# Optimization experiments

Hardware: AMD Instinct MI355X
Metric: run time of the kernel (lower is better)

## Reference

```python
import jax, jax.numpy as jnp
import numpy as np
from jax import lax

B, D, K = 65536, 256, 32  # batch, num_latent_dims, flow_depth


def setup_inputs() -> dict:
    key = jax.random.key(0)
    k1, k2, k3, k4, k5 = jax.random.split(key, 5)
    X = jax.random.normal(k1, (B, D), dtype=jnp.float32)
    h = jax.random.normal(k2, (B, D), dtype=jnp.float32)  # passed through, unused by planar math
    u = jax.random.normal(k3, (K, D), dtype=jnp.float32) * 0.1
    w = jax.random.normal(k4, (K, D), dtype=jnp.float32) * 0.1
    b = jax.random.normal(k5, (K,), dtype=jnp.float32) * 0.1
    return {"X": X, "h": h, "u": u, "w": w, "b": b}


def _planar_chain(z0, u, w, b):
    """Sequential planar normalizing flow: z_{k+1} = z_k + u_hat_k * tanh(w_k.z_k + b_k)."""

    def step(z, params):
        u_k, w_k, b_k = params  # (D,), (D,), scalar
        # enforce invertibility: u_hat so that w.u_hat >= -1
        wu = jnp.dot(w_k, u_k)
        u_hat = u_k + (jax.nn.softplus(wu) - 1.0 - wu) * w_k / jnp.dot(w_k, w_k)
        lin = z @ w_k + b_k              # (B,)
        t = jnp.tanh(lin)                # (B,)
        z_new = z + t[:, None] * u_hat[None, :]
        # psi = (1 - t^2) w ; log|det J| = log|1 + psi.u_hat|
        log_det = jnp.log(jnp.abs(1.0 + (1.0 - t * t) * jnp.dot(w_k, u_hat)) + 1e-8)
        return z_new, log_det

    z_final, log_dets = lax.scan(step, z0, (u, w, b))
    return z_final, log_dets  # (B, D), (K, B)


def reference(X, h, u, w, b):
    z = X.reshape(X.shape[0], X.shape[1])  # view(B, D, -1) then view(B, D) -> (B, D)
    z_final, log_det_jacobians = _planar_chain(z, u, w, b)
    return z_final, log_det_jacobians
```

## Files before the change

kernel.cpp:

```cpp
#include <hip/hip_runtime.h>


#define B_ 65536
#define D_ 256
#define ROWS 128
#define GRID (B_ / ROWS)

#define WS_WT 0
#define WS_UH 8192
#define WS_G  16384
#define WS_C  17408

#define P_STR 132
#define T_OFF 4224
#define G_OFF 8448
#define C_OFF 9504
#define BB_OFF 9536
#define LDS_FLOATS 9568

__global__ __launch_bounds__(256) void nf_gen(const float* __restrict__ u_in,
                                              const float* __restrict__ w_in,
                                              float* __restrict__ ws) {
  __shared__ float wTg[8192];
  __shared__ float ug[8192];
  __shared__ float wu_s[32], ww_s[32], coefs_s[32];
  const int t = threadIdx.x;
  {
    const int k = t & 31, d0 = (t >> 5) * 32;
    const float4* wp = (const float4*)(w_in + k * 256 + d0);
#pragma unroll
    for (int q = 0; q < 8; ++q) {
      float4 v = wp[q];
      wTg[(d0 + q * 4 + 0) * 32 + k] = v.x;
      wTg[(d0 + q * 4 + 1) * 32 + k] = v.y;
      wTg[(d0 + q * 4 + 2) * 32 + k] = v.z;
      wTg[(d0 + q * 4 + 3) * 32 + k] = v.w;
    }
#pragma unroll
    for (int q = 0; q < 8; ++q)
      ((float4*)ug)[t + 256 * q] = ((const float4*)u_in)[t + 256 * q];
  }
  __syncthreads();
  const int k = t & 31, jg = t >> 5;
  float m1[4] = {0.f, 0.f, 0.f, 0.f}, m2[4] = {0.f, 0.f, 0.f, 0.f};
#pragma unroll 4
  for (int dc = 0; dc < 64; ++dc) {
    float wk[4];
    float4 wj[4], uj[4];
#pragma unroll
    for (int i = 0; i < 4; ++i) wk[i] = wTg[(dc * 4 + i) * 32 + k];
#pragma unroll
    for (int i = 0; i < 4; ++i) wj[i] = *(const float4*)&wTg[(dc * 4 + i) * 32 + jg * 4];
#pragma unroll
    for (int i = 0; i < 4; ++i) uj[i] = *(const float4*)&ug[(jg * 4 + i) * 256 + dc * 4];
#pragma unroll
    for (int i = 0; i < 4; ++i) {
      m1[i] = fmaf(uj[i].x, wk[0], m1[i]);
      m1[i] = fmaf(uj[i].y, wk[1], m1[i]);
      m1[i] = fmaf(uj[i].z, wk[2], m1[i]);
      m1[i] = fmaf(uj[i].w, wk[3], m1[i]);
    }
    const float* w0 = (const float*)&wj[0];
    const float* w1 = (const float*)&wj[1];
    const float* w2 = (const float*)&wj[2];
    const float* w3 = (const float*)&wj[3];
#pragma unroll
    for (int i = 0; i < 4; ++i) {
      m2[i] = fmaf(w0[i], wk[0], m2[i]);
      m2[i] = fmaf(w1[i], wk[1], m2[i]);
      m2[i] = fmaf(w2[i], wk[2], m2[i]);
      m2[i] = fmaf(w3[i], wk[3], m2[i]);
    }
  }
  if ((k >> 2) == jg) {
    wu_s[k] = m1[k & 3];
    ww_s[k] = m2[k & 3];
  }
  __syncthreads();
  if (t < 32) {
    float wu = wu_s[t], ww = ww_s[t];
    float sp = fmaxf(wu, 0.f) + log1pf(__expf(-fabsf(wu)));
    coefs_s[t] = (sp - 1.f - wu) / ww;
    ws[WS_C + t] = sp - 1.f;
  }
  __syncthreads();
#pragma unroll
  for (int i = 0; i < 4; ++i)
    ws[WS_G + k * 32 + jg * 4 + i] = fmaf(coefs_s[jg * 4 + i], m2[i], m1[i]);
  {
    const int k2 = t >> 3, d0 = (t & 7) * 32;
    const float ck = coefs_s[k2];
    const float4* up = (const float4*)(u_in + k2 * 256 + d0);
    const float4* wp2 = (const float4*)(w_in + k2 * 256 + d0);
    float4* od = (float4*)(ws + WS_UH + k2 * 256 + d0);
#pragma unroll
    for (int q = 0; q < 8; ++q) {
      float4 uv = up[q], wv = wp2[q];
      uv.x = fmaf(ck, wv.x, uv.x);
      uv.y = fmaf(ck, wv.y, uv.y);
      uv.z = fmaf(ck, wv.z, uv.z);
      uv.w = fmaf(ck, wv.w, uv.w);
      od[q] = uv;
    }
  }
#pragma unroll
  for (int q = 0; q < 8; ++q)
    ((float4*)(ws + WS_WT))[t + 256 * q] = ((const float4*)wTg)[t + 256 * q];
}

__global__ __launch_bounds__(256) void nf_fused(const float* __restrict__ X,
                                                const float* __restrict__ b_in,
                                                const float* __restrict__ ws,
                                                float* __restrict__ out) {
  __shared__ float lds[LDS_FLOATS];

  const int t = threadIdx.x;
  const int row0 = blockIdx.x * ROWS;
  const int xoff = (t >> 6) * 32 + ((t >> 3) & 7) * 4;
  const int kq4 = (t & 7) * 4;
  const int cq8 = (t & 7) * 8;

  float p[4][4];
#pragma unroll
  for (int a = 0; a < 4; ++a)
#pragma unroll
    for (int b2 = 0; b2 < 4; ++b2) p[a][b2] = 0.f;
  {
    const float* wbase = ws + WS_WT + kq4;
    const float* xb = X + (size_t)(row0 + xoff) * 256;
#pragma unroll 2
    for (int dq = 0; dq < 64; ++dq) {
      float4 wr[4];
#pragma unroll
      for (int i = 0; i < 4; ++i) wr[i] = *(const float4*)(wbase + (dq * 4 + i) * 32);
      float4 xr[4];
#pragma unroll
      for (int a = 0; a < 4; ++a) xr[a] = *(const float4*)(xb + a * 256 + dq * 4);
#pragma unroll
      for (int a = 0; a < 4; ++a) {
        const float xf[4] = {xr[a].x, xr[a].y, xr[a].z, xr[a].w};
#pragma unroll
        for (int i = 0; i < 4; ++i) {
          p[a][0] = fmaf(xf[i], wr[i].x, p[a][0]);
          p[a][1] = fmaf(xf[i], wr[i].y, p[a][1]);
          p[a][2] = fmaf(xf[i], wr[i].z, p[a][2]);
          p[a][3] = fmaf(xf[i], wr[i].w, p[a][3]);
        }
      }
    }
  }

#pragma unroll
  for (int b2 = 0; b2 < 4; ++b2)
    *(float4*)&lds[(kq4 + b2) * P_STR + xoff] =
        make_float4(p[0][b2], p[1][b2], p[2][b2], p[3][b2]);
#pragma unroll
  for (int i = 0; i < 4; ++i) {
    const int e = t * 4 + i;
    lds[G_OFF + (e >> 5) * 33 + (e & 31)] = ws[WS_G + e];
  }
  if (t < 32) {
    lds[C_OFF + t] = ws[WS_C + t];
    lds[BB_OFF + t] = b_in[t];
  }
  __syncthreads();

  if (t < 128) {
    float pfull[32];
#pragma unroll
    for (int j = 0; j < 32; ++j) pfull[j] = lds[j * P_STR + t] + lds[BB_OFF + j];
    float tvv[32];
#pragma unroll
    for (int kk = 0; kk < 32; ++kk) {
      float la = pfull[kk], lb = 0.f;
      const float* gp = &lds[G_OFF + kk * 33];
#pragma unroll
      for (int j = 0; j + 1 < kk; j += 2) {
        la = fmaf(tvv[j], gp[j], la);
        lb = fmaf(tvv[j + 1], gp[j + 1], lb);
      }
      if (kk & 1) la = fmaf(tvv[kk - 1], gp[kk - 1], la);
      float lin = la + lb;
      float e = __expf(2.f * lin);
      float tk = 1.f - 2.f / (e + 1.f);
      tvv[kk] = tk;
      lds[T_OFF + kk * P_STR + t] = tk;
      float val = fabsf(fmaf(1.f - tk * tk, lds[C_OFF + kk], 1.f)) + 1e-8f;
      out[(size_t)B_ * D_ + (size_t)kk * B_ + row0 + t] = __logf(val);
    }
  }
  __syncthreads();

  for (int cbk = 0; cbk < 4; ++cbk) {
    const int c0 = cbk * 64 + cq8;
    float acc[4][8];
#pragma unroll
    for (int a = 0; a < 4; ++a) {
      const float4 x0 = *(const float4*)(X + (size_t)(row0 + xoff + a) * 256 + c0);
      const float4 x1 = *(const float4*)(X + (size_t)(row0 + xoff + a) * 256 + c0 + 4);
      acc[a][0] = x0.x; acc[a][1] = x0.y; acc[a][2] = x0.z; acc[a][3] = x0.w;
      acc[a][4] = x1.x; acc[a][5] = x1.y; acc[a][6] = x1.z; acc[a][7] = x1.w;
    }
#pragma unroll 4
    for (int kk = 0; kk < 32; ++kk) {
      float4 t4 = *(const float4*)&lds[T_OFF + kk * P_STR + xoff];
      float4 u0 = *(const float4*)(ws + WS_UH + kk * 256 + c0);
      float4 u1 = *(const float4*)(ws + WS_UH + kk * 256 + c0 + 4);
      const float tr[4] = {t4.x, t4.y, t4.z, t4.w};
      const float uk[8] = {u0.x, u0.y, u0.z, u0.w, u1.x, u1.y, u1.z, u1.w};
#pragma unroll
      for (int a = 0; a < 4; ++a)
#pragma unroll
        for (int b2 = 0; b2 < 8; ++b2) acc[a][b2] = fmaf(tr[a], uk[b2], acc[a][b2]);
    }
#pragma unroll
    for (int a = 0; a < 4; ++a) {
      float4* op = (float4*)(out + (size_t)(row0 + xoff + a) * 256 + c0);
      op[0] = make_float4(acc[a][0], acc[a][1], acc[a][2], acc[a][3]);
      op[1] = make_float4(acc[a][4], acc[a][5], acc[a][6], acc[a][7]);
    }
  }
}

extern "C" void kernel_launch(void* const* d_in, const int* in_sizes, int n_in,
                              void* d_out, int out_size, void* d_ws, size_t ws_size,
                              hipStream_t stream) {
  const float* X = (const float*)d_in[0];
  const float* u = (const float*)d_in[2];
  const float* w = (const float*)d_in[3];
  const float* b = (const float*)d_in[4];
  float* out = (float*)d_out;
  float* ws = (float*)d_ws;

  nf_gen<<<1, 256, 0, stream>>>(u, w, ws);
  nf_fused<<<GRID, 256, 0, stream>>>(X, b, ws, out);
}
```

Measured before the change: 223.8 us.

## Restructure fused planar flow kernel to 128 threads with LDS-staged X tiles

The fused kernel now runs with 128 threads per block. Each wave owns 16 flow columns and each lane owns 2 rows. X is staged through LDS in 32-column slabs using a swizzled transposed layout, with register prefetch of the next slab. The weight, G, coefficient and bias values are read directly from global memory as wave-uniform, likely scalar, loads instead of being copied into LDS. The aim is to cut redundant global X loads and LDS traffic, at the cost of fewer threads per block and many more accumulator registers, which may limit occupancy.

```diff
diff --git a/kernel.cpp b/kernel.cpp
--- a/kernel.cpp
+++ b/kernel.cpp
@@ -5,18 +5,16 @@
 #define D_ 256
 #define ROWS 128
 #define GRID (B_ / ROWS)
+#define NTHR 128
 
 #define WS_WT 0
 #define WS_UH 8192
 #define WS_G  16384
 #define WS_C  17408
 
-#define P_STR 132
-#define T_OFF 4224
-#define G_OFF 8448
-#define C_OFF 9504
-#define BB_OFF 9536
-#define LDS_FLOATS 9568
+#define XS 0
+#define TS 0
+#define PS 4096
 
 __global__ __launch_bounds__(256) void nf_gen(const float* __restrict__ u_in,
                                               const float* __restrict__ w_in,
@@ -108,72 +106,85 @@
     ((float4*)(ws + WS_WT))[t + 256 * q] = ((const float4*)wTg)[t + 256 * q];
 }
 
-__global__ __launch_bounds__(256) void nf_fused(const float* __restrict__ X,
-                                                const float* __restrict__ b_in,
-                                                const float* __restrict__ ws,
-                                                float* __restrict__ out) {
-  __shared__ float lds[LDS_FLOATS];
+__global__ __launch_bounds__(NTHR, 2) void nf_fused(const float* __restrict__ X,
+                                                    const float* __restrict__ b_in,
+                                                    const float* __restrict__ ws,
+                                                    float* __restrict__ out) {
+  __shared__ float lds[8192];
 
   const int t = threadIdx.x;
+  const int lane = t & 63;
+  const int wvu = __builtin_amdgcn_readfirstlane(t >> 6);
   const int row0 = blockIdx.x * ROWS;
-  const int xoff = (t >> 6) * 32 + ((t >> 3) & 7) * 4;
-  const int kq4 = (t & 7) * 4;
-  const int cq8 = (t & 7) * 8;
-
-  float p[4][4];
-#pragma unroll
-  for (int a = 0; a < 4; ++a)
-#pragma unroll
-    for (int b2 = 0; b2 < 4; ++b2) p[a][b2] = 0.f;
-  {
-    const float* wbase = ws + WS_WT + kq4;
-    const float* xb = X + (size_t)(row0 + xoff) * 256;
-#pragma unroll 2
-    for (int dq = 0; dq < 64; ++dq) {
-      float4 wr[4];
-#pragma unroll
-      for (int i = 0; i < 4; ++i) wr[i] = *(const float4*)(wbase + (dq * 4 + i) * 32);
-      float4 xr[4];
-#pragma unroll
-      for (int a = 0; a < 4; ++a) xr[a] = *(const float4*)(xb + a * 256 + dq * 4);
-#pragma unroll
-      for (int a = 0; a < 4; ++a) {
-        const float xf[4] = {xr[a].x, xr[a].y, xr[a].z, xr[a].w};
-#pragma unroll
-        for (int i = 0; i < 4; ++i) {
-          p[a][0] = fmaf(xf[i], wr[i].x, p[a][0]);
-          p[a][1] = fmaf(xf[i], wr[i].y, p[a][1]);
-          p[a][2] = fmaf(xf[i], wr[i].z, p[a][2]);
-          p[a][3] = fmaf(xf[i], wr[i].w, p[a][3]);
-        }
-      }
-    }
-  }
-
-#pragma unroll
-  for (int b2 = 0; b2 < 4; ++b2)
-    *(float4*)&lds[(kq4 + b2) * P_STR + xoff] =
-        make_float4(p[0][b2], p[1][b2], p[2][b2], p[3][b2]);
-#pragma unroll
-  for (int i = 0; i < 4; ++i) {
-    const int e = t * 4 + i;
-    lds[G_OFF + (e >> 5) * 33 + (e & 31)] = ws[WS_G + e];
-  }
-  if (t < 32) {
-    lds[C_OFF + t] = ws[WS_C + t];
-    lds[BB_OFF + t] = b_in[t];
-  }
-  __syncthreads();
-
-  if (t < 128) {
+  const int r2 = 2 * lane;
+  const int srow = t >> 2;
+  const int scol = (t & 3) * 8;
+
+  float4 pf[8];
+  auto load_stage = [&](int s) {
+#pragma unroll
+    for (int rp = 0; rp < 4; ++rp) {
+      const float* src = X + (size_t)(row0 + rp * 32 + srow) * 256 + s * 32 + scol;
+      pf[rp * 2 + 0] = ((const float4*)src)[0];
+      pf[rp * 2 + 1] = ((const float4*)src)[1];
+    }
+  };
+  auto store_stage = [&]() {
+#pragma unroll
+    for (int rp = 0; rp < 4; ++rp) {
+      const int row = rp * 32 + srow;
+      const float f[8] = {pf[rp * 2].x,     pf[rp * 2].y,     pf[rp * 2].z,
+                          pf[rp * 2].w,     pf[rp * 2 + 1].x, pf[rp * 2 + 1].y,
+                          pf[rp * 2 + 1].z, pf[rp * 2 + 1].w};
+#pragma unroll
+      for (int i = 0; i < 8; ++i) {
+        const int c = scol + i;
+        lds[XS + c * 128 + ((row + 6 * c) & 127)] = f[i];
+      }
+    }
+  };
+
+  float p0[16], p1[16];
+#pragma unroll
+  for (int i = 0; i < 16; ++i) { p0[i] = 0.f; p1[i] = 0.f; }
+
+  load_stage(0);
+  const float* wtab = ws + WS_WT + wvu * 16;
+  for (int s = 0; s < 8; ++s) {
+    store_stage();
+    __syncthreads();
+    if (s < 7) load_stage(s + 1);
+#pragma unroll 4
+    for (int dl = 0; dl < 32; ++dl) {
+      const int d = s * 32 + dl;
+      float2 xv = *(const float2*)&lds[XS + dl * 128 + ((r2 + 6 * dl) & 127)];
+      const float* wk = wtab + d * 32;
+#pragma unroll
+      for (int i = 0; i < 16; ++i) {
+        p0[i] = fmaf(xv.x, wk[i], p0[i]);
+        p1[i] = fmaf(xv.y, wk[i], p1[i]);
+      }
+    }
+    __syncthreads();
+  }
+
+  {
+    const int kb = wvu * 16;
+#pragma unroll
+    for (int i = 0; i < 16; ++i)
+      *(float2*)&lds[PS + (kb + i) * 128 + r2] = make_float2(p0[i], p1[i]);
+  }
+  __syncthreads();
+
+  {
     float pfull[32];
 #pragma unroll
-    for (int j = 0; j < 32; ++j) pfull[j] = lds[j * P_STR + t] + lds[BB_OFF + j];
+    for (int j = 0; j < 32; ++j) pfull[j] = lds[PS + j * 128 + t] + b_in[j];
     float tvv[32];
 #pragma unroll
     for (int kk = 0; kk < 32; ++kk) {
       float la = pfull[kk], lb = 0.f;
-      const float* gp = &lds[G_OFF + kk * 33];
+      const float* gp = ws + WS_G + kk * 32;
 #pragma unroll
       for (int j = 0; j + 1 < kk; j += 2) {
         la = fmaf(tvv[j], gp[j], la);
@@ -184,40 +195,48 @@
       float e = __expf(2.f * lin);
       float tk = 1.f - 2.f / (e + 1.f);
       tvv[kk] = tk;
-      lds[T_OFF + kk * P_STR + t] = tk;
-      float val = fabsf(fmaf(1.f - tk * tk, lds[C_OFF + kk], 1.f)) + 1e-8f;
+      lds[TS + kk * 128 + t] = tk;
+      float val = fabsf(fmaf(1.f - tk * tk, ws[WS_C + kk], 1.f)) + 1e-8f;
       out[(size_t)B_ * D_ + (size_t)kk * B_ + row0 + t] = __logf(val);
     }
   }
   __syncthreads();
 
-  for (int cbk = 0; cbk < 4; ++cbk) {
-    const int c0 = cbk * 64 + cq8;
-    float acc[4][8];
-#pragma unroll
-    for (int a = 0; a < 4; ++a) {
-      const float4 x0 = *(const float4*)(X + (size_t)(row0 + xoff + a) * 256 + c0);
-      const float4 x1 = *(const float4*)(X + (size_t)(row0 + xoff + a) * 256 + c0 + 4);
-      acc[a][0] = x0.x; acc[a][1] = x0.y; acc[a][2] = x0.z; acc[a][3] = x0.w;
-      acc[a][4] = x1.x; acc[a][5] = x1.y; acc[a][6] = x1.z; acc[a][7] = x1.w;
-    }
-#pragma unroll 4
+  const float* uws = ws + WS_UH;
+  for (int ps = 0; ps < 4; ++ps) {
+    const int c0 = ps * 64 + wvu * 32;
+    float a0[32], a1[32];
+    {
+      const float* x0 = X + (size_t)(row0 + r2) * 256 + c0;
+      const float* x1 = X + (size_t)(row0 + r2 + 1) * 256 + c0;
+#pragma unroll
+      for (int q = 0; q < 8; ++q) {
+        float4 v0 = ((const float4*)x0)[q];
+        float4 v1 = ((const float4*)x1)[q];
+        a0[q * 4 + 0] = v0.x; a0[q * 4 + 1] = v0.y;
+        a0[q * 4 + 2] = v0.z; a0[q * 4 + 3] = v0.w;
+        a1[q * 4 + 0] = v1.x; a1[q * 4 + 1] = v1.y;
+        a1[q * 4 + 2] = v1.z; a1[q * 4 + 3] = v1.w;
+      }
+    }
+#pragma unroll 2
     for (int kk = 0; kk < 32; ++kk) {
-      float4 t4 = *(const float4*)&lds[T_OFF + kk * P_STR + xoff];
-      float4 u0 = *(const float4*)(ws + WS_UH + kk * 256 + c0);
-      float4 u1 = *(const float4*)(ws + WS_UH + kk * 256 + c0 + 4);
-      const float tr[4] = {t4.x, t4.y, t4.z, t4.w};
-      const float uk[8] = {u0.x, u0.y, u0.z, u0.w, u1.x, u1.y, u1.z, u1.w};
-#pragma unroll
-      for (int a = 0; a < 4; ++a)
-#pragma unroll
-        for (int b2 = 0; b2 < 8; ++b2) acc[a][b2] = fmaf(tr[a], uk[b2], acc[a][b2]);
-    }
-#pragma unroll
-    for (int a = 0; a < 4; ++a) {
-      float4* op = (float4*)(out + (size_t)(row0 + xoff + a) * 256 + c0);
-      op[0] = make_float4(acc[a][0], acc[a][1], acc[a][2], acc[a][3]);
-      op[1] = make_float4(acc[a][4], acc[a][5], acc[a][6], acc[a][7]);
+      float2 tv = *(const float2*)&lds[TS + kk * 128 + r2];
+      const float* uk = uws + kk * 256 + c0;
+#pragma unroll
+      for (int c = 0; c < 32; ++c) {
+        a0[c] = fmaf(tv.x, uk[c], a0[c]);
+        a1[c] = fmaf(tv.y, uk[c], a1[c]);
+      }
+    }
+    {
+      float* o0 = out + (size_t)(row0 + r2) * 256 + c0;
+      float* o1 = out + (size_t)(row0 + r2 + 1) * 256 + c0;
+#pragma unroll
+      for (int q = 0; q < 8; ++q) {
+        ((float4*)o0)[q] = make_float4(a0[q * 4], a0[q * 4 + 1], a0[q * 4 + 2], a0[q * 4 + 3]);
+        ((float4*)o1)[q] = make_float4(a1[q * 4], a1[q * 4 + 1], a1[q * 4 + 2], a1[q * 4 + 3]);
+      }
     }
   }
 }
@@ -233,5 +252,5 @@
   float* ws = (float*)d_ws;
 
   nf_gen<<<1, 256, 0, stream>>>(u, w, ws);
-  nf_fused<<<GRID, 256, 0, stream>>>(X, b, ws, out);
+  nf_fused<<<GRID, NTHR, 0, stream>>>(X, b, ws, out);
 }
```

New measurement: 248.6 us. 11.1% more time.
